# Kernel tuning notes

Measured on AMD Instinct MI355X. Metric: run time of the kernel, lower is better.

Reference implementation:

```python
import jax, jax.numpy as jnp
import numpy as np

N_HEAD = 8
D_ATTN = 64
D_MODEL = 512


def setup_inputs() -> dict:
    key = jax.random.key(0)
    ks = jax.random.split(key, 12)
    B, S = 2, 2048
    inp = {
        "input": jax.random.normal(ks[0], (B, S, D_MODEL), dtype=jnp.float32),
        "top": jax.random.normal(ks[1], (B, S, S, 16), dtype=jnp.float32),
        # learned params (Linear: y = x @ W.T + b)
        "top_w": jax.random.normal(ks[2], (1, 16), dtype=jnp.float32) * 0.25,
        "top_b": jnp.zeros((1,), dtype=jnp.float32),
        "wq": jax.random.normal(ks[3], (N_HEAD * D_ATTN, D_MODEL), dtype=jnp.float32) * 0.02,
        "bq": jnp.zeros((N_HEAD * D_ATTN,), dtype=jnp.float32),
        "wk": jax.random.normal(ks[4], (N_HEAD * D_ATTN, D_MODEL), dtype=jnp.float32) * 0.02,
        "bk": jnp.zeros((N_HEAD * D_ATTN,), dtype=jnp.float32),
        "wv": jax.random.normal(ks[5], (N_HEAD * D_ATTN, D_MODEL), dtype=jnp.float32) * 0.02,
        "bv": jnp.zeros((N_HEAD * D_ATTN,), dtype=jnp.float32),
        "wo": jax.random.normal(ks[6], (D_MODEL, N_HEAD * D_ATTN), dtype=jnp.float32) * 0.02,
        "bo": jnp.zeros((D_MODEL,), dtype=jnp.float32),
    }
    return inp


def reference(input, top, top_w, top_b, wq, bq, wk, bk, wv, bv, wo, bo):
    B, S, _ = input.shape
    # pairwise topological bias: [B,S,S,16] @ [16,1] -> [B,S,S]
    bias = (jnp.einsum('bstf,f->bst', top, top_w[0]) + top_b[0])  # [B,S,S]
    bias = bias[:, None, :, :]  # broadcast over heads: [B,1,S,S]

    def proj(w, b):
        # [B,S,D] -> [B,H,S,d]
        return (input @ w.T + b).reshape(B, S, N_HEAD, D_ATTN).transpose(0, 2, 1, 3)

    Q, K, V = proj(wq, bq), proj(wk, bk), proj(wv, bv)
    scores = jnp.einsum('bhqd,bhkd->bhqk', Q, K) / jnp.sqrt(jnp.float32(D_ATTN))
    attn = jax.nn.softmax(scores + bias, axis=-1)
    O = jnp.einsum('bhqk,bhkd->bhqd', attn, V)  # [B,H,S,d]
    O = O.transpose(0, 2, 1, 3).reshape(B, S, N_HEAD * D_ATTN)
    return O @ wo.T + bo
```

## Files before the change

kernel.cpp:

```cpp
#include <hip/hip_runtime.h>
#include <hip/hip_bf16.h>
#include <math.h>

#define S_LEN 2048
#define BATCH 2
#define NH 8
#define DH 64
#define DM 512
#define LOG2E 1.44269504088896f

typedef __attribute__((ext_vector_type(8))) short short8;
typedef __attribute__((ext_vector_type(4))) float floatx4;

__device__ __forceinline__ unsigned short f2bf(float f) {
  union { float f; unsigned u; } v; v.f = f;
  unsigned r = v.u + 0x7FFFu + ((v.u >> 16) & 1u);
  return (unsigned short)(r >> 16);
}

__device__ __forceinline__ unsigned pkbf(float a, float b) {
  __hip_bfloat162 h = __float22bfloat162_rn(make_float2(a, b));
  union { __hip_bfloat162 h; unsigned u; } v; v.h = h;
  return v.u;
}

__global__ __launch_bounds__(256) void cvt_all(const float* __restrict__ in,
                                               const float* __restrict__ wq, const float* __restrict__ wk,
                                               const float* __restrict__ wv, const float* __restrict__ wo,
                                               unsigned short* __restrict__ in_bf,
                                               unsigned short* __restrict__ qw, unsigned short* __restrict__ kw,
                                               unsigned short* __restrict__ vw, unsigned short* __restrict__ ow) {
  int bid = blockIdx.x;
  const float* src; unsigned short* dst; int base;
  if (bid < 2048) { src = in; dst = in_bf; base = bid; }
  else {
    int wsel = (bid - 2048) >> 8;
    base = (bid - 2048) & 255;
    switch (wsel) {
      case 0: src = wq; dst = qw; break;
      case 1: src = wk; dst = kw; break;
      case 2: src = wv; dst = vw; break;
      default: src = wo; dst = ow; break;
    }
  }
  int i = base * 256 + threadIdx.x;
  float4 f = ((const float4*)src)[i];
  ((uint2*)dst)[i] = make_uint2(pkbf(f.x, f.y), pkbf(f.z, f.w));
}

__global__ __launch_bounds__(256) void bias_topo(const float* __restrict__ top,
                                                 const float* __restrict__ top_w,
                                                 const float* __restrict__ top_b,
                                                 float* __restrict__ bias) {
  size_t e = (size_t)blockIdx.x * blockDim.x + threadIdx.x;
  const float4* t = (const float4*)(top + e * 16);
  const float4* w = (const float4*)top_w;
  float acc = top_b[0];
#pragma unroll
  for (int j = 0; j < 4; j++) {
    float4 tv = t[j]; float4 wv = w[j];
    acc += tv.x * wv.x + tv.y * wv.y + tv.z * wv.z + tv.w * wv.w;
  }
  bias[e] = acc * LOG2E;
}

__global__ __launch_bounds__(256) void gemm_bt(const unsigned short* __restrict__ A,
                                               const unsigned short* __restrict__ W0,
                                               const unsigned short* __restrict__ W1,
                                               const unsigned short* __restrict__ W2,
                                               const float* __restrict__ b0, const float* __restrict__ b1,
                                               const float* __restrict__ b2,
                                               void* __restrict__ o0, void* __restrict__ o1, void* __restrict__ o2,
                                               int qkv, float scale0) {
  __shared__ unsigned short As[64][72];
  __shared__ unsigned short Ws[64][72];
  const int z = qkv ? blockIdx.z : 0;
  const unsigned short* W = (z == 0) ? W0 : (z == 1) ? W1 : W2;
  const float* bias = (z == 0) ? b0 : (z == 1) ? b1 : b2;
  void* out = (z == 0) ? o0 : (z == 1) ? o1 : o2;
  const int mode = qkv ? ((z == 2) ? 2 : 1) : 0;
  const float scale = (z == 0) ? scale0 : 1.0f;

  const int m0 = blockIdx.x * 64, n0 = blockIdx.y * 64;
  const int tid = threadIdx.x;
  const int w = tid >> 6, l = tid & 63;
  const int lr = l & 15, lg = l >> 4;

  floatx4 acc[4];
#pragma unroll
  for (int nb = 0; nb < 4; nb++)
#pragma unroll
    for (int i = 0; i < 4; i++) acc[nb][i] = 0.f;

  const int srow = tid >> 2;
  const int sseg = (tid & 3) * 16;

  for (int k0 = 0; k0 < 512; k0 += 64) {
    const unsigned short* ap = A + (size_t)(m0 + srow) * 512 + k0 + sseg;
    const unsigned short* wp = W + (size_t)(n0 + srow) * 512 + k0 + sseg;
    *(short8*)&As[srow][sseg]     = *(const short8*)ap;
    *(short8*)&As[srow][sseg + 8] = *(const short8*)(ap + 8);
    *(short8*)&Ws[srow][sseg]     = *(const short8*)wp;
    *(short8*)&Ws[srow][sseg + 8] = *(const short8*)(wp + 8);
    __syncthreads();
#pragma unroll
    for (int kk = 0; kk < 2; kk++) {
      short8 af = *(const short8*)&As[w * 16 + lr][kk * 32 + lg * 8];
#pragma unroll
      for (int nb = 0; nb < 4; nb++) {
        short8 bf = *(const short8*)&Ws[nb * 16 + lr][kk * 32 + lg * 8];
        acc[nb] = __builtin_amdgcn_mfma_f32_16x16x32_bf16(af, bf, acc[nb], 0, 0, 0);
      }
    }
    __syncthreads();
  }

  if (mode == 2) {
#pragma unroll
    for (int nb = 0; nb < 4; nb++) {
      const float bv = bias[n0 + nb * 16 + lr];
      unsigned lo = pkbf(acc[nb][0] + bv, acc[nb][1] + bv);
      unsigned hi = pkbf(acc[nb][2] + bv, acc[nb][3] + bv);
      *(uint2*)&As[nb * 16 + lr][w * 16 + lg * 4] = make_uint2(lo, hi);
    }
    __syncthreads();
    const int b = m0 >> 11, s_base = m0 & 2047;
    const int h = n0 >> 6;
    unsigned short* outp = (unsigned short*)out + (size_t)(b * 8 + h) * DH * S_LEN;
    const int row = tid >> 2, seg = (tid & 3) * 16;
    short8 v0 = *(const short8*)&As[row][seg];
    short8 v1 = *(const short8*)&As[row][seg + 8];
    *(short8*)(outp + (size_t)row * S_LEN + s_base + seg)     = v0;
    *(short8*)(outp + (size_t)row * S_LEN + s_base + seg + 8) = v1;
    return;
  }

#pragma unroll
  for (int nb = 0; nb < 4; nb++) {
    const int n = n0 + nb * 16 + lr;
    const float bv = bias[n];
#pragma unroll
    for (int i = 0; i < 4; i++) {
      const int m = m0 + w * 16 + lg * 4 + i;
      float v = (acc[nb][i] + bv) * scale;
      if (mode == 0) {
        ((float*)out)[(size_t)m * 512 + n] = v;
      } else {
        const int b = m >> 11, s = m & 2047;
        const int h = n >> 6, d = n & 63;
        ((unsigned short*)out)[((size_t)(b * 8 + h) * 2048 + s) * 64 + d] = f2bf(v);
      }
    }
  }
}

__global__ __launch_bounds__(256) void attn_kernel(const unsigned short* __restrict__ Qb,
                                                   const unsigned short* __restrict__ Kb,
                                                   const unsigned short* __restrict__ Vt,
                                                   const float* __restrict__ biasb,
                                                   unsigned short* __restrict__ Ob) {
  __shared__ unsigned short Ps[4][16][72];
  const int q0 = blockIdx.x * 64;
  const int bh = blockIdx.y;
  const int b = bh >> 3, h = bh & 7;
  const int tid = threadIdx.x;
  const int w = tid >> 6, l = tid & 63;
  const int lr = l & 15, lg = l >> 4;

  const unsigned short* Qh = Qb + (size_t)bh * S_LEN * DH;
  const unsigned short* Kh = Kb + (size_t)bh * S_LEN * DH;
  const unsigned short* Vh = Vt + (size_t)bh * DH * S_LEN;

  const int q = q0 + w * 16 + lr;
  short8 qf[2];
  qf[0] = *(const short8*)(Qh + (size_t)q * DH + lg * 8);
  qf[1] = *(const short8*)(Qh + (size_t)q * DH + 32 + lg * 8);

  float m_i = -1e30f, l_i = 0.f;
  floatx4 o[4];
#pragma unroll
  for (int nd = 0; nd < 4; nd++)
#pragma unroll
    for (int i = 0; i < 4; i++) o[nd][i] = 0.f;

  const float* brow = biasb + ((size_t)b * S_LEN + q) * S_LEN;

  for (int k0 = 0; k0 < S_LEN; k0 += 64) {
    floatx4 sa[4];
#pragma unroll
    for (int nb = 0; nb < 4; nb++)
#pragma unroll
      for (int i = 0; i < 4; i++) sa[nb][i] = 0.f;
    __builtin_amdgcn_s_setprio(1);
#pragma unroll
    for (int kk = 0; kk < 2; kk++) {
#pragma unroll
      for (int nb = 0; nb < 4; nb++) {
        short8 kf = *(const short8*)(Kh + (size_t)(k0 + nb * 16 + lr) * DH + kk * 32 + lg * 8);
        sa[nb] = __builtin_amdgcn_mfma_f32_16x16x32_bf16(kf, qf[kk], sa[nb], 0, 0, 0);
      }
    }
    __builtin_amdgcn_s_setprio(0);
    float p[4][4];
    float mx = -1e30f;
#pragma unroll
    for (int nb = 0; nb < 4; nb++) {
      float4 bv = *(const float4*)(brow + k0 + nb * 16 + lg * 4);
      p[nb][0] = sa[nb][0] + bv.x;
      p[nb][1] = sa[nb][1] + bv.y;
      p[nb][2] = sa[nb][2] + bv.z;
      p[nb][3] = sa[nb][3] + bv.w;
      mx = fmaxf(mx, fmaxf(fmaxf(p[nb][0], p[nb][1]), fmaxf(p[nb][2], p[nb][3])));
    }
    mx = fmaxf(mx, __shfl_xor(mx, 16));
    mx = fmaxf(mx, __shfl_xor(mx, 32));
    const float mnew = fmaxf(m_i, mx);
    const float alpha = exp2f(m_i - mnew);
    float rs = 0.f;
#pragma unroll
    for (int nb = 0; nb < 4; nb++)
#pragma unroll
      for (int i = 0; i < 4; i++) {
        p[nb][i] = exp2f(p[nb][i] - mnew);
        rs += p[nb][i];
      }
    rs += __shfl_xor(rs, 16);
    rs += __shfl_xor(rs, 32);
    l_i = l_i * alpha + rs;
    m_i = mnew;
#pragma unroll
    for (int nd = 0; nd < 4; nd++)
#pragma unroll
      for (int i = 0; i < 4; i++) o[nd][i] *= alpha;
#pragma unroll
    for (int nb = 0; nb < 4; nb++) {
      unsigned lo = pkbf(p[nb][0], p[nb][1]);
      unsigned hi = pkbf(p[nb][2], p[nb][3]);
      *(uint2*)&Ps[w][lr][nb * 16 + lg * 4] = make_uint2(lo, hi);
    }
    __builtin_amdgcn_s_setprio(1);
#pragma unroll
    for (int kk = 0; kk < 2; kk++) {
      short8 pf = *(const short8*)&Ps[w][lr][kk * 32 + lg * 8];
#pragma unroll
      for (int nd = 0; nd < 4; nd++) {
        short8 vf = *(const short8*)(Vh + (size_t)(nd * 16 + lr) * S_LEN + k0 + kk * 32 + lg * 8);
        o[nd] = __builtin_amdgcn_mfma_f32_16x16x32_bf16(vf, pf, o[nd], 0, 0, 0);
      }
    }
    __builtin_amdgcn_s_setprio(0);
  }

  const float inv = 1.0f / l_i;
#pragma unroll
  for (int nd = 0; nd < 4; nd++) {
    unsigned lo = pkbf(o[nd][0] * inv, o[nd][1] * inv);
    unsigned hi = pkbf(o[nd][2] * inv, o[nd][3] * inv);
    *(uint2*)(Ob + ((size_t)b * S_LEN + q) * DM + h * DH + nd * 16 + lg * 4) = make_uint2(lo, hi);
  }
}

extern "C" void kernel_launch(void* const* d_in, const int* in_sizes, int n_in,
                              void* d_out, int out_size, void* d_ws, size_t ws_size,
                              hipStream_t stream) {
  const float* input = (const float*)d_in[0];
  const float* top   = (const float*)d_in[1];
  const float* top_w = (const float*)d_in[2];
  const float* top_b = (const float*)d_in[3];
  const float* wq = (const float*)d_in[4];
  const float* bq = (const float*)d_in[5];
  const float* wk = (const float*)d_in[6];
  const float* bk = (const float*)d_in[7];
  const float* wv = (const float*)d_in[8];
  const float* bv = (const float*)d_in[9];
  const float* wo = (const float*)d_in[10];
  const float* bo = (const float*)d_in[11];

  char* ws = (char*)d_ws;
  float* bias_ws = (float*)ws;              ws += (size_t)BATCH * S_LEN * S_LEN * 4;
  unsigned short* in_bf = (unsigned short*)ws;  ws += (size_t)BATCH * S_LEN * DM * 2;
  unsigned short* wq_bf = (unsigned short*)ws;  ws += (size_t)DM * DM * 2;
  unsigned short* wk_bf = (unsigned short*)ws;  ws += (size_t)DM * DM * 2;
  unsigned short* wv_bf = (unsigned short*)ws;  ws += (size_t)DM * DM * 2;
  unsigned short* wo_bf = (unsigned short*)ws;  ws += (size_t)DM * DM * 2;
  unsigned short* qb  = (unsigned short*)ws;    ws += (size_t)BATCH * NH * S_LEN * DH * 2;
  unsigned short* kb  = (unsigned short*)ws;    ws += (size_t)BATCH * NH * S_LEN * DH * 2;
  unsigned short* vtb = (unsigned short*)ws;    ws += (size_t)BATCH * NH * S_LEN * DH * 2;
  unsigned short* ob  = (unsigned short*)ws;    ws += (size_t)BATCH * S_LEN * DM * 2;

  cvt_all<<<3072, 256, 0, stream>>>(input, wq, wk, wv, wo, in_bf, wq_bf, wk_bf, wv_bf, wo_bf);

  bias_topo<<<(BATCH * S_LEN * S_LEN) / 256, 256, 0, stream>>>(top, top_w, top_b, bias_ws);

  gemm_bt<<<dim3(4096 / 64, 512 / 64, 3), 256, 0, stream>>>(
      in_bf, wq_bf, wk_bf, wv_bf, bq, bk, bv, qb, kb, vtb, 1, 0.125f * LOG2E);

  attn_kernel<<<dim3(S_LEN / 64, BATCH * NH), 256, 0, stream>>>(qb, kb, vtb, bias_ws, ob);

  gemm_bt<<<dim3(4096 / 64, 512 / 64, 1), 256, 0, stream>>>(
      ob, wo_bf, nullptr, nullptr, bo, nullptr, nullptr, d_out, nullptr, nullptr, 0, 1.0f);
}
```

Before: 875.9 us.

## Fuse topo-bias reduction into QKV GEMM launch and defer softmax rescaling

Merges the bias_topo kernel into the QKV projection launch as extra blocks, so the memory-bound bias reduction (reading the large top tensor) can run alongside the compute-bound GEMM blocks. Each bias block now handles four chunks and loads the weights once. The output projection gets its own specialised gemm_bt without mode branches. In attention, the running-max update and rescaling of o/l are skipped when the new tile max stays within 8 (log2 units) of the current max. This saves exp and multiply work but lets unnormalised values grow to about 2^8, which bf16 and fp32 can hold.

```diff
diff --git a/kernel.cpp b/kernel.cpp
--- a/kernel.cpp
+++ b/kernel.cpp
@@ -48,41 +48,54 @@
   ((uint2*)dst)[i] = make_uint2(pkbf(f.x, f.y), pkbf(f.z, f.w));
 }
 
-__global__ __launch_bounds__(256) void bias_topo(const float* __restrict__ top,
-                                                 const float* __restrict__ top_w,
-                                                 const float* __restrict__ top_b,
-                                                 float* __restrict__ bias) {
-  size_t e = (size_t)blockIdx.x * blockDim.x + threadIdx.x;
-  const float4* t = (const float4*)(top + e * 16);
-  const float4* w = (const float4*)top_w;
-  float acc = top_b[0];
-#pragma unroll
-  for (int j = 0; j < 4; j++) {
-    float4 tv = t[j]; float4 wv = w[j];
-    acc += tv.x * wv.x + tv.y * wv.y + tv.z * wv.z + tv.w * wv.w;
-  }
-  bias[e] = acc * LOG2E;
-}
-
-__global__ __launch_bounds__(256) void gemm_bt(const unsigned short* __restrict__ A,
-                                               const unsigned short* __restrict__ W0,
-                                               const unsigned short* __restrict__ W1,
-                                               const unsigned short* __restrict__ W2,
-                                               const float* __restrict__ b0, const float* __restrict__ b1,
-                                               const float* __restrict__ b2,
-                                               void* __restrict__ o0, void* __restrict__ o1, void* __restrict__ o2,
-                                               int qkv, float scale0) {
+#define GEMM_BLKS 1536
+#define BIAS_BLKS 8192
+__global__ __launch_bounds__(256) void qkv_bias_fused(const unsigned short* __restrict__ A,
+                                                      const unsigned short* __restrict__ W0,
+                                                      const unsigned short* __restrict__ W1,
+                                                      const unsigned short* __restrict__ W2,
+                                                      const float* __restrict__ b0, const float* __restrict__ b1,
+                                                      const float* __restrict__ b2,
+                                                      void* __restrict__ o0, void* __restrict__ o1, void* __restrict__ o2,
+                                                      float scale0,
+                                                      const float* __restrict__ top,
+                                                      const float* __restrict__ top_w,
+                                                      const float* __restrict__ top_b,
+                                                      float* __restrict__ bias_out) {
   __shared__ unsigned short As[64][72];
   __shared__ unsigned short Ws[64][72];
-  const int z = qkv ? blockIdx.z : 0;
+  const int bid = blockIdx.x;
+  const int tid = threadIdx.x;
+
+  if (bid >= GEMM_BLKS) {
+    const int bb = bid - GEMM_BLKS;
+    const float4* wv4 = (const float4*)top_w;
+    const float4 w0 = wv4[0], w1 = wv4[1], w2 = wv4[2], w3 = wv4[3];
+    const float tb = top_b[0];
+#pragma unroll
+    for (int it = 0; it < 4; ++it) {
+      const size_t e = ((size_t)(bb + it * BIAS_BLKS)) * 256 + tid;
+      const float4* t = (const float4*)(top + e * 16);
+      const float4 t0 = t[0], t1 = t[1], t2 = t[2], t3 = t[3];
+      float acc = tb;
+      acc += t0.x * w0.x + t0.y * w0.y + t0.z * w0.z + t0.w * w0.w;
+      acc += t1.x * w1.x + t1.y * w1.y + t1.z * w1.z + t1.w * w1.w;
+      acc += t2.x * w2.x + t2.y * w2.y + t2.z * w2.z + t2.w * w2.w;
+      acc += t3.x * w3.x + t3.y * w3.y + t3.z * w3.z + t3.w * w3.w;
+      bias_out[e] = acc * LOG2E;
+    }
+    return;
+  }
+
+  const int z = bid >> 9;
+  const int r = bid & 511;
+  const int m0 = (r & 63) * 64, n0 = (r >> 6) * 64;
   const unsigned short* W = (z == 0) ? W0 : (z == 1) ? W1 : W2;
   const float* bias = (z == 0) ? b0 : (z == 1) ? b1 : b2;
   void* out = (z == 0) ? o0 : (z == 1) ? o1 : o2;
-  const int mode = qkv ? ((z == 2) ? 2 : 1) : 0;
+  const int mode = (z == 2) ? 2 : 1;
   const float scale = (z == 0) ? scale0 : 1.0f;
 
-  const int m0 = blockIdx.x * 64, n0 = blockIdx.y * 64;
-  const int tid = threadIdx.x;
   const int w = tid >> 6, l = tid & 63;
   const int lr = l & 15, lg = l >> 4;
 
@@ -143,13 +156,61 @@
     for (int i = 0; i < 4; i++) {
       const int m = m0 + w * 16 + lg * 4 + i;
       float v = (acc[nb][i] + bv) * scale;
-      if (mode == 0) {
-        ((float*)out)[(size_t)m * 512 + n] = v;
-      } else {
-        const int b = m >> 11, s = m & 2047;
-        const int h = n >> 6, d = n & 63;
-        ((unsigned short*)out)[((size_t)(b * 8 + h) * 2048 + s) * 64 + d] = f2bf(v);
-      }
+      const int b = m >> 11, s = m & 2047;
+      const int h = n >> 6, d = n & 63;
+      ((unsigned short*)out)[((size_t)(b * 8 + h) * 2048 + s) * 64 + d] = f2bf(v);
+    }
+  }
+}
+
+__global__ __launch_bounds__(256) void gemm_bt(const unsigned short* __restrict__ A,
+                                               const unsigned short* __restrict__ W0,
+                                               const float* __restrict__ b0,
+                                               float* __restrict__ o0) {
+  __shared__ unsigned short As[64][72];
+  __shared__ unsigned short Ws[64][72];
+  const int m0 = blockIdx.x * 64, n0 = blockIdx.y * 64;
+  const int tid = threadIdx.x;
+  const int w = tid >> 6, l = tid & 63;
+  const int lr = l & 15, lg = l >> 4;
+
+  floatx4 acc[4];
+#pragma unroll
+  for (int nb = 0; nb < 4; nb++)
+#pragma unroll
+    for (int i = 0; i < 4; i++) acc[nb][i] = 0.f;
+
+  const int srow = tid >> 2;
+  const int sseg = (tid & 3) * 16;
+
+  for (int k0 = 0; k0 < 512; k0 += 64) {
+    const unsigned short* ap = A + (size_t)(m0 + srow) * 512 + k0 + sseg;
+    const unsigned short* wp = W0 + (size_t)(n0 + srow) * 512 + k0 + sseg;
+    *(short8*)&As[srow][sseg]     = *(const short8*)ap;
+    *(short8*)&As[srow][sseg + 8] = *(const short8*)(ap + 8);
+    *(short8*)&Ws[srow][sseg]     = *(const short8*)wp;
+    *(short8*)&Ws[srow][sseg + 8] = *(const short8*)(wp + 8);
+    __syncthreads();
+#pragma unroll
+    for (int kk = 0; kk < 2; kk++) {
+      short8 af = *(const short8*)&As[w * 16 + lr][kk * 32 + lg * 8];
+#pragma unroll
+      for (int nb = 0; nb < 4; nb++) {
+        short8 bf = *(const short8*)&Ws[nb * 16 + lr][kk * 32 + lg * 8];
+        acc[nb] = __builtin_amdgcn_mfma_f32_16x16x32_bf16(af, bf, acc[nb], 0, 0, 0);
+      }
+    }
+    __syncthreads();
+  }
+
+#pragma unroll
+  for (int nb = 0; nb < 4; nb++) {
+    const int n = n0 + nb * 16 + lr;
+    const float bv = b0[n];
+#pragma unroll
+    for (int i = 0; i < 4; i++) {
+      const int m = m0 + w * 16 + lg * 4 + i;
+      o0[(size_t)m * 512 + n] = acc[nb][i] + bv;
     }
   }
 }
@@ -214,24 +275,28 @@
     }
     mx = fmaxf(mx, __shfl_xor(mx, 16));
     mx = fmaxf(mx, __shfl_xor(mx, 32));
-    const float mnew = fmaxf(m_i, mx);
-    const float alpha = exp2f(m_i - mnew);
+    const bool defer = (__all(mx <= m_i + 8.f) != 0);
+    if (!defer) {
+      const float mnew = fmaxf(m_i, mx);
+      const float alpha = exp2f(m_i - mnew);
+      l_i *= alpha;
+#pragma unroll
+      for (int nd = 0; nd < 4; nd++)
+#pragma unroll
+        for (int i = 0; i < 4; i++) o[nd][i] *= alpha;
+      m_i = mnew;
+    }
     float rs = 0.f;
 #pragma unroll
     for (int nb = 0; nb < 4; nb++)
 #pragma unroll
       for (int i = 0; i < 4; i++) {
-        p[nb][i] = exp2f(p[nb][i] - mnew);
+        p[nb][i] = exp2f(p[nb][i] - m_i);
         rs += p[nb][i];
       }
     rs += __shfl_xor(rs, 16);
     rs += __shfl_xor(rs, 32);
-    l_i = l_i * alpha + rs;
-    m_i = mnew;
-#pragma unroll
-    for (int nd = 0; nd < 4; nd++)
-#pragma unroll
-      for (int i = 0; i < 4; i++) o[nd][i] *= alpha;
+    l_i += rs;
 #pragma unroll
     for (int nb = 0; nb < 4; nb++) {
       unsigned lo = pkbf(p[nb][0], p[nb][1]);
@@ -290,13 +355,11 @@
 
   cvt_all<<<3072, 256, 0, stream>>>(input, wq, wk, wv, wo, in_bf, wq_bf, wk_bf, wv_bf, wo_bf);
 
-  bias_topo<<<(BATCH * S_LEN * S_LEN) / 256, 256, 0, stream>>>(top, top_w, top_b, bias_ws);
-
-  gemm_bt<<<dim3(4096 / 64, 512 / 64, 3), 256, 0, stream>>>(
-      in_bf, wq_bf, wk_bf, wv_bf, bq, bk, bv, qb, kb, vtb, 1, 0.125f * LOG2E);
+  qkv_bias_fused<<<GEMM_BLKS + BIAS_BLKS, 256, 0, stream>>>(
+      in_bf, wq_bf, wk_bf, wv_bf, bq, bk, bv, qb, kb, vtb, 0.125f * LOG2E,
+      top, top_w, top_b, bias_ws);
 
   attn_kernel<<<dim3(S_LEN / 64, BATCH * NH), 256, 0, stream>>>(qb, kb, vtb, bias_ws, ob);
 
-  gemm_bt<<<dim3(4096 / 64, 512 / 64, 1), 256, 0, stream>>>(
-      ob, wo_bf, nullptr, nullptr, bo, nullptr, nullptr, d_out, nullptr, nullptr, 0, 1.0f);
-}
+  gemm_bt<<<dim3(4096 / 64, 512 / 64), 256, 0, stream>>>(ob, wo_bf, bo, (float*)d_out);
+}
```

After: 877.2 us. Within noise of the previous version (+0.1%).
